# Kernel optimization log

Hardware: AMD Instinct MI355X
Metric: run time of the kernel (lower is better)

## Reference

```python
import jax, jax.numpy as jnp
import numpy as np

N = 100_000          # nodes
E = 3_200_000        # edges (avg degree 32)
NEG_SLOPE = 0.2      # PyG GATConv default


def _gat_conv(x, src, dst, W, a_src, a_dst, b, n):
    """Single-head PyG-style GATConv. src/dst already include self-loops."""
    h = x @ W                                   # [N, F_out]
    logits = (h @ a_src)[src] + (h @ a_dst)[dst]  # [E']
    e = jax.nn.leaky_relu(logits, NEG_SLOPE)
    m = jax.ops.segment_max(e, dst, num_segments=n)
    ex = jnp.exp(e - m[dst])                    # stable ragged softmax over in-edges
    s = jax.ops.segment_sum(ex, dst, num_segments=n)
    alpha = ex / (s[dst] + 1e-16)
    out = jax.ops.segment_sum(h[src] * alpha[:, None], dst, num_segments=n)
    return out + b


def setup_inputs() -> dict:
    key = jax.random.key(0)
    ks = jax.random.split(key, 20)
    x = jax.random.normal(ks[0], (N, 3), dtype=jnp.float32)
    edge_index = jax.random.randint(ks[1], (2, E), 0, N, dtype=jnp.int64)

    def lin(k, fin, fout):
        return jax.random.normal(k, (fin, fout), dtype=jnp.float32) * (1.0 / np.sqrt(fin))

    def att(k, f):
        return jax.random.normal(k, (f,), dtype=jnp.float32) * (1.0 / np.sqrt(f))

    inp = {"x": x, "edge_index": edge_index}
    # forward-direction convs
    inp["W1"], inp["as1"], inp["ad1"], inp["b1"] = lin(ks[2], 3, 16), att(ks[3], 16), att(ks[4], 16), jnp.zeros((16,), jnp.float32)
    inp["W2"], inp["as2"], inp["ad2"], inp["b2"] = lin(ks[5], 16, 1), att(ks[6], 1), att(ks[7], 1), jnp.zeros((1,), jnp.float32)
    # reverse-direction convs
    inp["W1r"], inp["as1r"], inp["ad1r"], inp["b1r"] = lin(ks[8], 3, 16), att(ks[9], 16), att(ks[10], 16), jnp.zeros((16,), jnp.float32)
    inp["W2r"], inp["as2r"], inp["ad2r"], inp["b2r"] = lin(ks[11], 16, 1), att(ks[12], 1), att(ks[13], 1), jnp.zeros((1,), jnp.float32)
    return inp


def reference(x, edge_index, W1, as1, ad1, b1, W2, as2, ad2, b2,
              W1r, as1r, ad1r, b1r, W2r, as2r, ad2r, b2r):
    n = x.shape[0]
    loops = jnp.arange(n, dtype=edge_index.dtype)
    # forward direction (self-loops appended, as PyG add_self_loops=True)
    src = jnp.concatenate([edge_index[0], loops])
    dst = jnp.concatenate([edge_index[1], loops])
    # reverse direction: stack([ei[1], ei[0]]) then self-loops
    rsrc = jnp.concatenate([edge_index[1], loops])
    rdst = jnp.concatenate([edge_index[0], loops])

    xf = jax.nn.relu(_gat_conv(x, src, dst, W1, as1, ad1, b1, n))
    xf = _gat_conv(xf, src, dst, W2, as2, ad2, b2, n)

    xr = jax.nn.relu(_gat_conv(x, rsrc, rdst, W1r, as1r, ad1r, b1r, n))
    xr = _gat_conv(xr, rsrc, rdst, W2r, as2r, ad2r, b2r, n)

    return (xf + xr) * 0.5
```

## Files before the change

### kernel.cpp

```cpp
#include <hip/hip_runtime.h>
#include <math.h>

#define NSLOPE 0.2f
#define BSH 8
#define BNODES 256
#define NID_MASK 0x1FFFF
#define SENT 0xFFFFFFFFu
#define CAP 10240
#define GB 768
#define RE 2560
#define EPT 5
#define SLOT 12
#define SPILLCAP 256
#define BN9 512
#define LCAP 17408
#define BAGT 1024
#define CPP9 9

__device__ __forceinline__ float lrelu(float v) { return v > 0.f ? v : NSLOPE * v; }

__global__ void k_prep(const float* __restrict__ x,
                       const float* __restrict__ as1, const float* __restrict__ ad1,
                       const float* __restrict__ as1r, const float* __restrict__ ad1r,
                       const float* __restrict__ W1, const float* __restrict__ W1r,
                       float4* __restrict__ rec4f, float4* __restrict__ rec4r,
                       float* __restrict__ s1df, float* __restrict__ s1dr,
                       int* __restrict__ gcur, int NS, int N) {
    int i = blockIdx.x * blockDim.x + threadIdx.x;
    if (i < NS) gcur[i] = 0;
    if (i >= N) return;
    float x0 = x[3 * i], x1 = x[3 * i + 1], x2 = x[3 * i + 2];
    float ssf = 0.f, sdf = 0.f, ssr = 0.f, sdr = 0.f;
#pragma unroll
    for (int k = 0; k < 16; k++) {
        float hf = x0 * W1[k] + x1 * W1[16 + k] + x2 * W1[32 + k];
        ssf += hf * as1[k];
        sdf += hf * ad1[k];
        float hr = x0 * W1r[k] + x1 * W1r[16 + k] + x2 * W1r[32 + k];
        ssr += hr * as1r[k];
        sdr += hr * ad1r[k];
    }
    rec4f[i] = make_float4(x0, x1, x2, ssf);
    rec4r[i] = make_float4(x0, x1, x2, ssr);
    s1df[i] = sdf; s1dr[i] = sdr;
}

__global__ void __launch_bounds__(512) k_scatsort(
        const void* __restrict__ ei, long long E,
        int NB, int NS, int* __restrict__ gcur, unsigned* __restrict__ bin) {
    extern __shared__ unsigned smem[];
    unsigned* slots = smem;
    int* cnt  = (int*)(slots + (size_t)NS * SLOT);
    int* gpos = cnt + NS;
    int* spill_s = gpos + NS;
    int* spill_p = spill_s + SPILLCAP;
    unsigned* spill_r = (unsigned*)(spill_p + SPILLCAP);
    int* spn = (int*)(spill_r + SPILLCAP);
    __shared__ int flagsm;

    int t = threadIdx.x;
    if (t < 64) {
        const unsigned long long* p = (const unsigned long long*)ei;
        bool bad = false;
#pragma unroll
        for (int i = 0; i < 4; i++)
            if (p[t * 4 + i] >= (1ull << 32)) bad = true;
        unsigned long long mask = __ballot(bad);
        if (t == 0) flagsm = (mask == 0ull) ? 1 : 0;
    }
    __syncthreads();
    int fl = flagsm;
    long long chunk = (E + GB - 1) / GB;
    long long cstart = (long long)blockIdx.x * chunk;
    long long cend = cstart + chunk; if (cend > E) cend = E;

    for (long long rs = cstart; rs < cend; rs += RE) {
        int ne = (int)min((long long)RE, cend - rs);
        for (int c = t; c < NS; c += 512) cnt[c] = 0;
        if (t == 0) *spn = 0;
        int eu[EPT], ev[EPT];
#pragma unroll
        for (int k = 0; k < EPT; k++) {
            int idx = t + k * 512;
            eu[k] = -1;
            if (idx < ne) {
                long long i = rs + idx;
                if (fl) { const long long* p = (const long long*)ei;
                          eu[k] = (int)p[i]; ev[k] = (int)p[E + i]; }
                else    { const int* p = (const int*)ei;
                          eu[k] = p[i]; ev[k] = p[E + i]; }
            }
        }
        __syncthreads();
#pragma unroll
        for (int k = 0; k < EPT; k++) {
            if (eu[k] >= 0) {
                int u = eu[k], v = ev[k];
                unsigned r0 = (unsigned)u | ((unsigned)(v & (BNODES - 1)) << 17);
                int s0 = v >> BSH;
                unsigned r1 = (unsigned)v | ((unsigned)(u & (BNODES - 1)) << 17);
                int s1 = NB + (u >> BSH);
                int p0 = atomicAdd(&cnt[s0], 1);
                if (p0 < SLOT) slots[s0 * SLOT + p0] = r0;
                else { int sp = atomicAdd(spn, 1); if (sp < SPILLCAP) { spill_s[sp] = s0; spill_p[sp] = p0; spill_r[sp] = r0; } }
                int p1 = atomicAdd(&cnt[s1], 1);
                if (p1 < SLOT) slots[s1 * SLOT + p1] = r1;
                else { int sp = atomicAdd(spn, 1); if (sp < SPILLCAP) { spill_s[sp] = s1; spill_p[sp] = p1; spill_r[sp] = r1; } }
            }
        }
        __syncthreads();
        for (int c = t; c < NS; c += 512) {
            int n = cnt[c];
            gpos[c] = n ? atomicAdd(&gcur[c], n) : 0;
        }
        __syncthreads();
        for (int c = t; c < NS; c += 512) {
            int n = cnt[c];
            if (!n) continue;
            int g = gpos[c];
            long long b = (long long)c * CAP;
            int m = n < SLOT ? n : SLOT;
            if (g + n <= CAP) {
                int j = 0;
                if (g & 1) { bin[b + g] = slots[c * SLOT]; j = 1; }
                for (; j + 2 <= m; j += 2)
                    *(uint2*)(bin + b + g + j) =
                        make_uint2(slots[c * SLOT + j], slots[c * SLOT + j + 1]);
                if (j < m) bin[b + g + j] = slots[c * SLOT + j];
            }
        }
        int nsp = *spn; if (nsp > SPILLCAP) nsp = SPILLCAP;
        for (int i = t; i < nsp; i += 512) {
            int s = spill_s[i];
            int off = gpos[s] + spill_p[i];
            if (off < CAP) bin[(long long)s * CAP + off] = spill_r[i];
        }
        __syncthreads();
    }
}

__global__ void __launch_bounds__(BAGT, 8) k_bagg1(
        unsigned* __restrict__ bin, const int* __restrict__ gcur,
        const float4* __restrict__ rec4f, const float* __restrict__ s1df,
        const float4* __restrict__ rec4r, const float* __restrict__ s1dr,
        const float* __restrict__ b1, const float* __restrict__ W1,
        const float* __restrict__ W2,
        const float* __restrict__ as2, const float* __restrict__ ad2,
        const float* __restrict__ b1r, const float* __restrict__ W1r,
        const float* __restrict__ W2r,
        const float* __restrict__ as2r, const float* __restrict__ ad2r,
        float2* __restrict__ p2f, float* __restrict__ s2df,
        float2* __restrict__ p2r, float* __restrict__ s2dr,
        int* __restrict__ aoff, int* __restrict__ aend, int NB8, int N) {
    int bb = blockIdx.x, dir = blockIdx.y;
    const float4* rec4 = dir ? rec4r : rec4f;
    const float* s1d = dir ? s1dr : s1df;
    const float* b1_ = dir ? b1r : b1;
    const float* W1_ = dir ? W1r : W1;
    const float* W2_ = dir ? W2r : W2;
    float as2v = dir ? as2r[0] : as2[0];
    float ad2v = dir ? ad2r[0] : ad2[0];
    float2* p2 = dir ? p2r : p2f;
    float* s2d = dir ? s2dr : s2df;

    int c0 = dir * NB8 + 2 * bb;
    bool c1ok = (2 * bb + 1) < NB8;
    long long base = (long long)c0 * CAP;
    int n0 = gcur[c0]; if (n0 > CAP) n0 = CAP;
    int n1 = c1ok ? gcur[c0 + 1] : 0; if (n1 > CAP) n1 = CAP;
    int np0 = (n0 + 1) >> 1, np1 = (n1 + 1) >> 1;
    if (np0 > LCAP / 2) np0 = LCAP / 2;
    if (np0 + np1 > LCAP / 2) np1 = LCAP / 2 - np0;
    int nptot = np0 + np1;
    int v0 = bb << 9;
    int nv = N - v0; if (nv > BN9) nv = BN9;

    __shared__ int cnt[BN9];
    __shared__ int loff[BN9];
    __shared__ int segtot[8];
    __shared__ unsigned lds_u[LCAP];
    int t = threadIdx.x;

    const uint2* bp0 = (const uint2*)(bin + base);
    const uint2* bp1 = (const uint2*)(bin + base) + CAP / 2;
    uint2 recs[CPP9];
#pragma unroll
    for (int k = 0; k < CPP9; k++) {
        int i = t + k * BAGT;
        uint2 r = make_uint2(SENT, SENT);
        if (i < np0) {
            r = bp0[i];
            if (2 * i + 1 >= n0) r.y = SENT;
        } else if (i < nptot) {
            int i1 = i - np0;
            r = bp1[i1];
            if (2 * i1 + 1 >= n1) r.y = SENT;
            r.x += (256u << 17);
            if (r.y != SENT) r.y += (256u << 17);
        }
        recs[k] = r;
    }
    if (t < BN9) cnt[t] = 0;
    __syncthreads();
#pragma unroll
    for (int k = 0; k < CPP9; k++) {
        if (recs[k].x != SENT) atomicAdd(&cnt[recs[k].x >> 17], 1);
        if (recs[k].y != SENT) atomicAdd(&cnt[recs[k].y >> 17], 1);
    }
    __syncthreads();
    if (t < BN9) {
        int lane = t & 63, wv = t >> 6;
        int val = cnt[t];
        int incl = val;
#pragma unroll
        for (int od = 1; od < 64; od <<= 1) {
            int up = __shfl_up(incl, od);
            if (lane >= od) incl += up;
        }
        if (lane == 63) segtot[wv] = incl;
        loff[t] = incl - val;
    }
    __syncthreads();
    if (t < BN9) {
        int wv = t >> 6;
        int offs = 0;
#pragma unroll
        for (int j = 0; j < 8; j++) offs += (j < wv) ? segtot[j] : 0;
        int ex = loff[t] + offs;
        loff[t] = ex;
        cnt[t] = ex;
    }
    __syncthreads();
#pragma unroll
    for (int k = 0; k < CPP9; k++) {
        if (recs[k].x != SENT) {
            int q = atomicAdd(&cnt[recs[k].x >> 17], 1);
            lds_u[q] = recs[k].x & NID_MASK;
        }
        if (recs[k].y != SENT) {
            int q = atomicAdd(&cnt[recs[k].y >> 17], 1);
            lds_u[q] = recs[k].y & NID_MASK;
        }
    }
    __syncthreads();
    int node = t >> 1, lane = t & 1;
    float sdv = (node < nv) ? s1d[v0 + node] : 0.f;
    float d = 0.f, a0 = 0.f, a1 = 0.f, a2 = 0.f;
    if (node < nv) {
        int ls = loff[node], le = cnt[node];
        for (int pos = ls + lane; pos < le; pos += 2) {
            unsigned u = lds_u[pos];
            float4 r = rec4[u];
            float w = __expf(lrelu(r.w + sdv));
            d += w; a0 += w * r.x; a1 += w * r.y; a2 += w * r.z;
        }
    }
    d  += __shfl_xor(d, 1);
    a0 += __shfl_xor(a0, 1);
    a1 += __shfl_xor(a1, 1);
    a2 += __shfl_xor(a2, 1);
    if (lane == 0 && node < nv) {
        int v = v0 + node;
        float4 r = rec4[v];
        float w = __expf(lrelu(r.w + sdv));
        float dd = d + w;
        float inv = 1.f / (dd + 1e-16f);
        float m0 = (a0 + w * r.x) * inv;
        float m1 = (a1 + w * r.y) * inv;
        float m2 = (a2 + w * r.z) * inv;
        float h2v = 0.f;
#pragma unroll
        for (int k = 0; k < 16; k++) {
            float o = m0 * W1_[k] + m1 * W1_[16 + k] + m2 * W1_[32 + k] + b1_[k];
            o = fmaxf(o, 0.f);
            h2v += o * W2_[k];
        }
        p2[v] = make_float2(h2v, h2v * as2v);
        s2d[v] = h2v * ad2v;
    }
    int nreal = (nv > 0) ? cnt[nv - 1] : 0;
    if (t == 0 && (nreal & 1)) lds_u[nreal] = SENT;
    __syncthreads();
    int ndp = (nreal + 1) >> 1;
    uint2* bq = (uint2*)(bin + base);
    for (int i = t; i < ndp; i += BAGT)
        bq[i] = make_uint2(lds_u[2 * i], lds_u[2 * i + 1]);
    if (t < nv) {
        aoff[dir * N + v0 + t] = (int)(base + loff[t]);
        aend[dir * N + v0 + t] = (int)(base + cnt[t]);
    }
}

__global__ void k_agg2(const unsigned* __restrict__ bin,
                       const int* __restrict__ aoff, const int* __restrict__ aend,
                       const float2* __restrict__ p2f, const float* __restrict__ s2df,
                       const float2* __restrict__ p2r, const float* __restrict__ s2dr,
                       const float* __restrict__ b2, const float* __restrict__ b2r,
                       float* __restrict__ out, int N) {
    int tid = blockIdx.x * blockDim.x + threadIdx.x;
    int v = tid >> 4;
    int lane = tid & 15;
    if (v >= N) return;
    float res[2];
#pragma unroll
    for (int dir = 0; dir < 2; dir++) {
        const float2* p2 = dir ? p2r : p2f;
        const float* s2d = dir ? s2dr : s2df;
        float bias = dir ? b2r[0] : b2[0];
        float sd = s2d[v];
        int st = aoff[dir * N + v], en = aend[dir * N + v];
        float d = 0.f, a = 0.f;
        if (lane == 0) {
            float2 ts = p2[v];
            float w = __expf(lrelu(ts.y + sd));
            d = w; a = w * ts.x;
        }
        int j = st + lane;
        for (; j + 16 < en; j += 32) {
            unsigned u0 = __builtin_nontemporal_load(bin + j);
            unsigned u1 = __builtin_nontemporal_load(bin + j + 16);
            float2 t0 = p2[u0];
            float2 t1 = p2[u1];
            float w0 = __expf(lrelu(t0.y + sd));
            float w1 = __expf(lrelu(t1.y + sd));
            d += w0 + w1;
            a += w0 * t0.x + w1 * t1.x;
        }
        for (; j < en; j += 16) {
            unsigned u = __builtin_nontemporal_load(bin + j);
            float2 t = p2[u];
            float w = __expf(lrelu(t.y + sd));
            d += w;
            a += w * t.x;
        }
#pragma unroll
        for (int mask = 1; mask < 16; mask <<= 1) {
            d += __shfl_xor(d, mask);
            a += __shfl_xor(a, mask);
        }
        res[dir] = a / (d + 1e-16f) + bias;
    }
    if (lane == 0) out[v] = 0.5f * (res[0] + res[1]);
}

extern "C" void kernel_launch(void* const* d_in, const int* in_sizes, int n_in,
                              void* d_out, int out_size, void* d_ws, size_t ws_size,
                              hipStream_t stream) {
    const float* x   = (const float*)d_in[0];
    const void*  ei  = d_in[1];
    const float* W1  = (const float*)d_in[2];
    const float* as1 = (const float*)d_in[3];
    const float* ad1 = (const float*)d_in[4];
    const float* b1  = (const float*)d_in[5];
    const float* W2  = (const float*)d_in[6];
    const float* as2 = (const float*)d_in[7];
    const float* ad2 = (const float*)d_in[8];
    const float* b2  = (const float*)d_in[9];
    const float* W1r  = (const float*)d_in[10];
    const float* as1r = (const float*)d_in[11];
    const float* ad1r = (const float*)d_in[12];
    const float* b1r  = (const float*)d_in[13];
    const float* W2r  = (const float*)d_in[14];
    const float* as2r = (const float*)d_in[15];
    const float* ad2r = (const float*)d_in[16];
    const float* b2r  = (const float*)d_in[17];

    const int N = in_sizes[0] / 3;
    const long long E = in_sizes[1] / 2;
    const int NB8 = (N + BNODES - 1) >> BSH;
    const int NS = 2 * NB8;
    const int NB9 = (N + BN9 - 1) >> 9;

    char* w = (char*)d_ws;
    size_t o = 0;
    auto A = [&](size_t bytes) { o = (o + 255) & ~(size_t)255; size_t r = o; o += bytes; return r; };
    size_t oR4f  = A(sizeof(float4) * N);
    size_t oR4r  = A(sizeof(float4) * N);
    size_t oS1df = A(sizeof(float) * N);
    size_t oS1dr = A(sizeof(float) * N);
    size_t oP2f  = A(sizeof(float2) * N);
    size_t oS2df = A(sizeof(float) * N);
    size_t oP2r  = A(sizeof(float2) * N);
    size_t oS2dr = A(sizeof(float) * N);
    size_t oAoff = A(sizeof(int) * 2 * N);
    size_t oAend = A(sizeof(int) * 2 * N);
    size_t oGcur = A(sizeof(int) * NS);
    size_t oBin  = A(sizeof(unsigned) * (size_t)NS * CAP);
    (void)ws_size; (void)n_in; (void)out_size;

    float4* rec4f = (float4*)(w + oR4f);
    float4* rec4r = (float4*)(w + oR4r);
    float*  s1df = (float*)(w + oS1df);
    float*  s1dr = (float*)(w + oS1dr);
    float2* p2f  = (float2*)(w + oP2f);
    float*  s2df = (float*)(w + oS2df);
    float2* p2r  = (float2*)(w + oP2r);
    float*  s2dr = (float*)(w + oS2dr);
    int*    aoff = (int*)(w + oAoff);
    int*    aend = (int*)(w + oAend);
    int*    gcur = (int*)(w + oGcur);
    unsigned* bin = (unsigned*)(w + oBin);

    dim3 gN((N + 255) / 256);
    dim3 gAgg1(NB9, 2);
    dim3 gAgg2((N * 16 + 255) / 256);

    size_t smem = sizeof(unsigned) * (size_t)NS * SLOT
                + sizeof(int) * (size_t)NS * 2
                + sizeof(int) * SPILLCAP * 2
                + sizeof(unsigned) * SPILLCAP
                + 64;

    k_prep<<<gN, 256, 0, stream>>>(x, as1, ad1, as1r, ad1r, W1, W1r,
                                   rec4f, rec4r, s1df, s1dr, gcur, NS, N);
    k_scatsort<<<GB, 512, smem, stream>>>(ei, E, NB8, NS, gcur, bin);
    k_bagg1<<<gAgg1, BAGT, 0, stream>>>(bin, gcur, rec4f, s1df, rec4r, s1dr,
                                        b1, W1, W2, as2, ad2,
                                        b1r, W1r, W2r, as2r, ad2r,
                                        p2f, s2df, p2r, s2dr, aoff, aend, NB8, N);
    k_agg2<<<gAgg2, 256, 0, stream>>>(bin, aoff, aend, p2f, s2df, p2r, s2dr,
                                      b2, b2r, (float*)d_out, N);
}
```

Baseline: 231.3 us.

## Replace fixed-slot bucket scatter with count-scan-place local sort in scatter kernel

The edge bucketing kernel now does a two-pass local counting sort per round: it first counts records per bucket, runs a block-wide prefix scan to get contiguous shared-memory offsets, then places records and flushes each bucket's run to global memory with uint4/uint2 vectorized stores. This replaces the fixed 12-slot-per-bucket layout with its spill path, removes the size limits that could drop records, and allows larger rounds (more edges per thread, fewer blocks). A per-block rotation of the flush order spreads global atomics and writes across buckets. The cost is an extra counting pass plus a scan with several block syncs per round.

```diff
diff --git a/kernel.cpp b/kernel.cpp
--- a/kernel.cpp
+++ b/kernel.cpp
@@ -7,11 +7,11 @@
 #define NID_MASK 0x1FFFF
 #define SENT 0xFFFFFFFFu
 #define CAP 10240
-#define GB 768
-#define RE 2560
-#define EPT 5
-#define SLOT 12
-#define SPILLCAP 256
+#define GB2 512
+#define RT 512
+#define EPT2 13
+#define REDG (RT * EPT2)
+#define RREC (2 * REDG)
 #define BN9 512
 #define LCAP 17408
 #define BAGT 1024
@@ -45,17 +45,15 @@
     s1df[i] = sdf; s1dr[i] = sdr;
 }
 
-__global__ void __launch_bounds__(512) k_scatsort(
+__global__ void __launch_bounds__(RT) k_scatsort(
         const void* __restrict__ ei, long long E,
         int NB, int NS, int* __restrict__ gcur, unsigned* __restrict__ bin) {
     extern __shared__ unsigned smem[];
-    unsigned* slots = smem;
-    int* cnt  = (int*)(slots + (size_t)NS * SLOT);
-    int* gpos = cnt + NS;
-    int* spill_s = gpos + NS;
-    int* spill_p = spill_s + SPILLCAP;
-    unsigned* spill_r = (unsigned*)(spill_p + SPILLCAP);
-    int* spn = (int*)(spill_r + SPILLCAP);
+    unsigned* rec = smem;
+    int* cnt  = (int*)(rec + RREC);
+    int* loff = cnt + NS;
+    int* gbs  = loff + NS;
+    int* wtot = gbs + NS;
     __shared__ int flagsm;
 
     int t = threadIdx.x;
@@ -70,18 +68,18 @@
     }
     __syncthreads();
     int fl = flagsm;
-    long long chunk = (E + GB - 1) / GB;
+    long long chunk = (E + GB2 - 1) / GB2;
     long long cstart = (long long)blockIdx.x * chunk;
     long long cend = cstart + chunk; if (cend > E) cend = E;
-
-    for (long long rs = cstart; rs < cend; rs += RE) {
-        int ne = (int)min((long long)RE, cend - rs);
-        for (int c = t; c < NS; c += 512) cnt[c] = 0;
-        if (t == 0) *spn = 0;
-        int eu[EPT], ev[EPT];
-#pragma unroll
-        for (int k = 0; k < EPT; k++) {
-            int idx = t + k * 512;
+    int rot = (int)((blockIdx.x * 197u) % (unsigned)NS);
+
+    for (long long rs = cstart; rs < cend; rs += REDG) {
+        int ne = (int)min((long long)REDG, cend - rs);
+        for (int i = t; i < NS; i += RT) cnt[i] = 0;
+        int eu[EPT2], ev[EPT2];
+#pragma unroll
+        for (int k = 0; k < EPT2; k++) {
+            int idx = t + k * RT;
             eu[k] = -1;
             if (idx < ne) {
                 long long i = rs + idx;
@@ -93,47 +91,80 @@
         }
         __syncthreads();
 #pragma unroll
-        for (int k = 0; k < EPT; k++) {
+        for (int k = 0; k < EPT2; k++) {
+            if (eu[k] >= 0) {
+                atomicAdd(&cnt[ev[k] >> BSH], 1);
+                atomicAdd(&cnt[NB + (eu[k] >> BSH)], 1);
+            }
+        }
+        __syncthreads();
+        int base = 0;
+        for (int st = 0; st < NS; st += RT) {
+            int idx = st + t;
+            int val = (idx < NS) ? cnt[idx] : 0;
+            int lane = t & 63, wv = t >> 6;
+            int incl = val;
+#pragma unroll
+            for (int od = 1; od < 64; od <<= 1) {
+                int up = __shfl_up(incl, od);
+                if (lane >= od) incl += up;
+            }
+            if (lane == 63) wtot[wv] = incl;
+            __syncthreads();
+            int woff = 0;
+#pragma unroll
+            for (int j = 0; j < 8; j++) woff += (j < wv) ? wtot[j] : 0;
+            if (idx < NS) {
+                int lo = base + woff + incl - val;
+                loff[idx] = lo;
+                cnt[idx] = lo;
+                gbs[idx] = val ? atomicAdd(&gcur[idx], val) : 0;
+            }
+            int stot = 0;
+#pragma unroll
+            for (int j = 0; j < 8; j++) stot += wtot[j];
+            base += stot;
+            __syncthreads();
+        }
+#pragma unroll
+        for (int k = 0; k < EPT2; k++) {
             if (eu[k] >= 0) {
                 int u = eu[k], v = ev[k];
                 unsigned r0 = (unsigned)u | ((unsigned)(v & (BNODES - 1)) << 17);
                 int s0 = v >> BSH;
+                int p0 = atomicAdd(&cnt[s0], 1);
+                rec[p0] = r0;
                 unsigned r1 = (unsigned)v | ((unsigned)(u & (BNODES - 1)) << 17);
                 int s1 = NB + (u >> BSH);
-                int p0 = atomicAdd(&cnt[s0], 1);
-                if (p0 < SLOT) slots[s0 * SLOT + p0] = r0;
-                else { int sp = atomicAdd(spn, 1); if (sp < SPILLCAP) { spill_s[sp] = s0; spill_p[sp] = p0; spill_r[sp] = r0; } }
                 int p1 = atomicAdd(&cnt[s1], 1);
-                if (p1 < SLOT) slots[s1 * SLOT + p1] = r1;
-                else { int sp = atomicAdd(spn, 1); if (sp < SPILLCAP) { spill_s[sp] = s1; spill_p[sp] = p1; spill_r[sp] = r1; } }
+                rec[p1] = r1;
             }
         }
         __syncthreads();
-        for (int c = t; c < NS; c += 512) {
-            int n = cnt[c];
-            gpos[c] = n ? atomicAdd(&gcur[c], n) : 0;
-        }
-        __syncthreads();
-        for (int c = t; c < NS; c += 512) {
-            int n = cnt[c];
+        for (int i = t; i < NS; i += RT) {
+            int s = i + rot; if (s >= NS) s -= NS;
+            int ls = loff[s], le = cnt[s];
+            int n = le - ls;
             if (!n) continue;
-            int g = gpos[c];
-            long long b = (long long)c * CAP;
-            int m = n < SLOT ? n : SLOT;
-            if (g + n <= CAP) {
-                int j = 0;
-                if (g & 1) { bin[b + g] = slots[c * SLOT]; j = 1; }
-                for (; j + 2 <= m; j += 2)
-                    *(uint2*)(bin + b + g + j) =
-                        make_uint2(slots[c * SLOT + j], slots[c * SLOT + j + 1]);
-                if (j < m) bin[b + g + j] = slots[c * SLOT + j];
-            }
-        }
-        int nsp = *spn; if (nsp > SPILLCAP) nsp = SPILLCAP;
-        for (int i = t; i < nsp; i += 512) {
-            int s = spill_s[i];
-            int off = gpos[s] + spill_p[i];
-            if (off < CAP) bin[(long long)s * CAP + off] = spill_r[i];
+            int g = gbs[s];
+            if (g >= CAP) continue;
+            if (g + n > CAP) n = CAP - g;
+            long long b = (long long)s * CAP;
+            int j = 0;
+            if (g & 1) { bin[b + g] = rec[ls]; j = 1; }
+            if (((g + j) & 2) && j + 2 <= n) {
+                *(uint2*)(bin + b + g + j) = make_uint2(rec[ls + j], rec[ls + j + 1]);
+                j += 2;
+            }
+            for (; j + 4 <= n; j += 4)
+                *(uint4*)(bin + b + g + j) =
+                    make_uint4(rec[ls + j], rec[ls + j + 1],
+                               rec[ls + j + 2], rec[ls + j + 3]);
+            if (j + 2 <= n) {
+                *(uint2*)(bin + b + g + j) = make_uint2(rec[ls + j], rec[ls + j + 1]);
+                j += 2;
+            }
+            if (j < n) bin[b + g + j] = rec[ls + j];
         }
         __syncthreads();
     }
@@ -405,15 +436,14 @@
     dim3 gAgg1(NB9, 2);
     dim3 gAgg2((N * 16 + 255) / 256);
 
-    size_t smem = sizeof(unsigned) * (size_t)NS * SLOT
-                + sizeof(int) * (size_t)NS * 2
-                + sizeof(int) * SPILLCAP * 2
-                + sizeof(unsigned) * SPILLCAP
+    size_t smem = sizeof(unsigned) * (size_t)RREC
+                + sizeof(int) * (size_t)NS * 3
+                + sizeof(int) * 8
                 + 64;
 
     k_prep<<<gN, 256, 0, stream>>>(x, as1, ad1, as1r, ad1r, W1, W1r,
                                    rec4f, rec4r, s1df, s1dr, gcur, NS, N);
-    k_scatsort<<<GB, 512, smem, stream>>>(ei, E, NB8, NS, gcur, bin);
+    k_scatsort<<<GB2, RT, smem, stream>>>(ei, E, NB8, NS, gcur, bin);
     k_bagg1<<<gAgg1, BAGT, 0, stream>>>(bin, gcur, rec4f, s1df, rec4r, s1dr,
                                         b1, W1, W2, as2, ad2,
                                         b1r, W1r, W2r, as2r, ad2r,
```

Result: no change. 229.0 us (-1.0%).
